# Kernel tuning notes

Hardware: AMD Instinct MI355X
Metric: run time of the kernel (lower is better)

The kernel has to match this reference:

```python
import jax, jax.numpy as jnp
import numpy as np

N_NODES = 100000
N_EDGES = 1600000
IN_CH = 128
HID_CH = 128
OUT_CH = 64
N_GRAPHS = 256


def setup_inputs() -> dict:
    key = jax.random.key(0)
    ks = jax.random.split(key, 12)
    x = jax.random.normal(ks[0], (N_NODES, IN_CH), dtype=jnp.float32)
    edge_index = jax.random.randint(ks[1], (2, N_EDGES), 0, N_NODES, dtype=jnp.int64)
    batch = jnp.sort(jax.random.randint(ks[2], (N_NODES,), 0, N_GRAPHS, dtype=jnp.int64))
    def lin(k, fin, fout):
        bound = 1.0 / np.sqrt(fin)
        kw, kb = jax.random.split(k)
        W = jax.random.uniform(kw, (fin, fout), minval=-bound, maxval=bound, dtype=jnp.float32)
        b = jax.random.uniform(kb, (fout,), minval=-bound, maxval=bound, dtype=jnp.float32)
        return W, b
    W1, b1 = lin(ks[3], IN_CH, HID_CH)
    W2, b2 = lin(ks[4], HID_CH, HID_CH)
    W3, b3 = lin(ks[5], HID_CH, HID_CH)
    Wf, bf = lin(ks[6], HID_CH, OUT_CH)
    return {"x": x, "edge_index": edge_index, "batch": batch,
            "W1": W1, "b1": b1, "W2": W2, "b2": b2,
            "W3": W3, "b3": b3, "Wf": Wf, "bf": bf}


def _gin_conv(x, src, dst, W, b):
    # GINConv with eps=0: nn((1+eps)*x + sum_{j in N(i)} x_j)
    agg = jax.ops.segment_sum(x[src], dst, num_segments=N_NODES)
    return (x + agg) @ W + b


def reference(x, edge_index, batch, W1, b1, W2, b2, W3, b3, Wf, bf):
    src, dst = edge_index[0], edge_index[1]  # source_to_target flow
    h = jax.nn.relu(_gin_conv(x, src, dst, W1, b1))
    h = jax.nn.relu(_gin_conv(h, src, dst, W2, b2))
    h = jax.nn.relu(_gin_conv(h, src, dst, W3, b3))
    # global_mean_pool over graph ids
    sums = jax.ops.segment_sum(h, batch, num_segments=N_GRAPHS)  # [G, H]
    counts = jax.ops.segment_sum(jnp.ones((h.shape[0],), h.dtype), batch, num_segments=N_GRAPHS)
    pooled = sums / jnp.maximum(counts, 1.0)[:, None]
    # dropout is identity in eval mode
    logits = pooled @ Wf + bf  # [G, OUT_CH]
    return logits
```

## Files before the change

### kernel.cpp

```cpp
#include <hip/hip_runtime.h>

#define N_NODES 100000
#define N_EDGES 1600000
#define N_GRAPHS 256
#define CH 128
#define OUT_CH 64
#define NB 391
#define BCAP 4608
#define CAPN 48

typedef __attribute__((ext_vector_type(8))) short bf16x8;
typedef __attribute__((ext_vector_type(4))) float f32x4;
typedef __attribute__((ext_vector_type(2))) float f32x2;
typedef unsigned short ushort_t;
typedef unsigned int uint_t;
typedef unsigned char u8_t;

static __device__ inline ushort_t f2bf(float f) {
    uint_t u = __float_as_uint(f);
    uint_t r = (u + 0x7FFFu + ((u >> 16) & 1u)) >> 16;
    return (ushort_t)r;
}
static __device__ inline uint_t pack2bf(float x, float y) {
    return (uint_t)f2bf(x) | ((uint_t)f2bf(y) << 16);
}

static __device__ inline uint_t pack4fp8(float a, float b, float c, float d) {
    int v = __builtin_amdgcn_cvt_pk_fp8_f32(a, b, 0, false);
    v = __builtin_amdgcn_cvt_pk_fp8_f32(c, d, v, true);
    return (uint_t)v;
}
static __device__ inline u8_t f2fp8(float a) {
    return (u8_t)(__builtin_amdgcn_cvt_pk_fp8_f32(a, a, 0, false) & 0xFF);
}


__global__ __launch_bounds__(1024) void k_passA(const int* __restrict__ src, const int* __restrict__ dst,
                                                int* __restrict__ resCnt, uint_t* __restrict__ pairBuf,
                                                const float* __restrict__ x, u8_t* __restrict__ xb,
                                                const float* __restrict__ W1, const float* __restrict__ W2,
                                                const float* __restrict__ W3, ushort_t* __restrict__ WT) {
    int blk = blockIdx.x, tid = threadIdx.x;
    if (blk < 196) {
        __shared__ int hist[NB];
        __shared__ int base[NB];
        for (int t = tid; t < NB; t += 1024) hist[t] = 0;
        __syncthreads();
        uint_t v[8]; int bk[8], rk[8];
        int e0 = blk * 8192;
        #pragma unroll
        for (int j = 0; j < 8; ++j) {
            int e = e0 + j * 1024 + tid;
            bk[j] = -1;
            if (e < N_EDGES) {
                int d = dst[e];
                int s = src[e];
                int b = d >> 8;
                bk[j] = b;
                v[j] = (uint_t)s | ((uint_t)(d & 255) << 17);
                rk[j] = atomicAdd(&hist[b], 1);
            }
        }
        __syncthreads();
        for (int t = tid; t < NB; t += 1024)
            base[t] = atomicAdd(&resCnt[t * 16], hist[t]);
        __syncthreads();
        #pragma unroll
        for (int j = 0; j < 8; ++j) {
            if (bk[j] >= 0) {
                int pos = base[bk[j]] + rk[j];
                if (pos < BCAP) pairBuf[(size_t)bk[j] * BCAP + pos] = v[j];
            }
        }
    } else if (blk < 1759) {
        int i = (blk - 196) * 1024 + tid;
        if (i < N_NODES * 16) {
            const float4* xp = (const float4*)(x) + (size_t)i * 2;
            float4 a = xp[0], bb = xp[1];
            uint2 o;
            o.x = pack4fp8(a.x, a.y, a.z, a.w);
            o.y = pack4fp8(bb.x, bb.y, bb.z, bb.w);
            ((uint2*)xb)[i] = o;
        }
    } else {
        int idx = (blk - 1759) * 1024 + tid;
        int w = idx >> 14;
        int r = idx & 16383;
        const float* W = (w == 0) ? W1 : (w == 1) ? W2 : W3;
        int k = r >> 7, n = r & 127;
        WT[w * 16384 + n * 128 + k] = f2bf(W[r]);
    }
}


__global__ __launch_bounds__(256) void k_passB(const int* __restrict__ resCnt,
                                               const uint_t* __restrict__ pairBuf,
                                               int* __restrict__ cnt, int* __restrict__ col) {
    __shared__ int csr[256 * CAPN];
    __shared__ int lcnt[256];
    int b = blockIdx.x, tid = threadIdx.x;
    lcnt[tid] = 0;
    for (int i = tid; i < 256 * CAPN; i += 256) csr[i] = 0;
    __syncthreads();
    int ce = resCnt[b * 16];
    if (ce > BCAP) ce = BCAP;
    const uint_t* __restrict__ pb = pairBuf + (size_t)b * BCAP;
    for (int i = tid; i < ce; i += 256) {
        uint_t v = pb[i];
        int d = v >> 17;
        int p = atomicAdd(&lcnt[d], 1);
        if (p < CAPN) csr[d * CAPN + p] = (int)(v & 0x1FFFFu);
    }
    __syncthreads();
    int gbase = b * 256;
    int lim = (gbase + 256 <= N_NODES) ? 256 * CAPN : (N_NODES - gbase) * CAPN;
    for (int i = tid; i < lim; i += 256) col[(size_t)gbase * CAPN + i] = csr[i];
    int node = gbase + tid;
    if (node < N_NODES) {
        int c = lcnt[tid];
        cnt[node] = c > CAPN ? CAPN : c;
    }
}


__global__ __launch_bounds__(1024) void k_sort(const int* __restrict__ cnt, int* __restrict__ perm) {
    __shared__ int hist[CAPN + 1];
    __shared__ int base[CAPN + 1];
    int tid = threadIdx.x;
    if (tid <= CAPN) hist[tid] = 0;
    __syncthreads();
    for (int i = tid; i < N_NODES; i += 1024) atomicAdd(&hist[cnt[i]], 1);
    __syncthreads();
    if (tid == 0) {
        int s = 0;
        for (int b = 0; b <= CAPN; ++b) { base[b] = s; s += hist[b]; }
    }
    __syncthreads();
    for (int i = tid; i < N_NODES; i += 1024) {
        int p = atomicAdd(&base[cnt[i]], 1);
        perm[p] = i;
    }
}


__global__ __launch_bounds__(256) void k_fused(const u8_t* __restrict__ hin,
                                               const int* __restrict__ cnt,
                                               const int* __restrict__ col,
                                               const ushort_t* __restrict__ WT,
                                               const float* __restrict__ bias,
                                               u8_t* __restrict__ Hout,
                                               float* __restrict__ pooled,
                                               const int* __restrict__ batch,
                                               const int* __restrict__ perm) {
    __shared__ uint_t ldsZ[16][68];
    __shared__ float ldsO[16][132];
    __shared__ int ldsP[16];

    int tid  = threadIdx.x;
    int w    = tid >> 6;
    int lane = tid & 63;
    int row0 = blockIdx.x * 16;

    int mrow  = lane & 15;
    int kbase = (lane >> 4) * 8;
    int qid   = lane >> 4;
    int sl    = lane & 15;
    int qb    = qid * 16;

    if (tid < 16) ldsP[tid] = perm ? perm[row0 + tid] : (row0 + tid);

    int prow = row0 + w * 4 + qid;
    int node = perm ? perm[prow] : prow;
    int e = cnt[node];
    int cr0 = col[(size_t)node * CAPN + sl];
    int cr1 = (e > 16) ? col[(size_t)node * CAPN + 16 + sl] : 0;
    int cr2 = (e > 32) ? col[(size_t)node * CAPN + 32 + sl] : 0;

    int emax = e;
    emax = max(emax, __shfl(emax, lane ^ 16));
    emax = max(emax, __shfl(emax, lane ^ 32));

    float f0, f1, f2, f3, f4, f5, f6, f7;
    {
        uint2 sv = *(const uint2*)(hin + (size_t)node * 128 + sl * 8);
        f32x2 p0 = __builtin_amdgcn_cvt_pk_f32_fp8((int)sv.x, false);
        f32x2 p1 = __builtin_amdgcn_cvt_pk_f32_fp8((int)sv.x, true);
        f32x2 p2 = __builtin_amdgcn_cvt_pk_f32_fp8((int)sv.y, false);
        f32x2 p3 = __builtin_amdgcn_cvt_pk_f32_fp8((int)sv.y, true);
        f0 = p0.x; f1 = p0.y; f2 = p1.x; f3 = p1.y;
        f4 = p2.x; f5 = p2.y; f6 = p3.x; f7 = p3.y;
    }

#define ACCG(G, V)                                                       \
    {                                                                    \
        f32x2 p0 = __builtin_amdgcn_cvt_pk_f32_fp8((int)(V).x, false);   \
        f32x2 p1 = __builtin_amdgcn_cvt_pk_f32_fp8((int)(V).x, true);    \
        f32x2 p2 = __builtin_amdgcn_cvt_pk_f32_fp8((int)(V).y, false);   \
        f32x2 p3 = __builtin_amdgcn_cvt_pk_f32_fp8((int)(V).y, true);    \
        f0 = fmaf(G, p0.x, f0); f1 = fmaf(G, p0.y, f1);                  \
        f2 = fmaf(G, p1.x, f2); f3 = fmaf(G, p1.y, f3);                  \
        f4 = fmaf(G, p2.x, f4); f5 = fmaf(G, p2.y, f5);                  \
        f6 = fmaf(G, p3.x, f6); f7 = fmaf(G, p3.y, f7);                  \
    }

#define CHUNK(CREG, BASE)                                                    \
    if ((BASE) < emax) {                                                     \
        int lim = emax - (BASE); if (lim > 16) lim = 16;                     \
        for (int tt = 0; tt < lim; tt += 4) {                                \
            int i1 = tt + 1, i2 = tt + 2, i3 = tt + 3;                       \
            if (i1 > 15) i1 = 15; if (i2 > 15) i2 = 15; if (i3 > 15) i3 = 15;\
            int c0 = __shfl(CREG, qb + tt);                                  \
            int c1 = __shfl(CREG, qb + i1);                                  \
            int c2 = __shfl(CREG, qb + i2);                                  \
            int c3 = __shfl(CREG, qb + i3);                                  \
            bool v0 = (BASE) + tt     < e;                                   \
            bool v1 = (BASE) + tt + 1 < e;                                   \
            bool v2 = (BASE) + tt + 2 < e;                                   \
            bool v3 = (BASE) + tt + 3 < e;                                   \
            int a0 = v0 ? c0 : node;                                         \
            int a1 = v1 ? c1 : node;                                         \
            int a2 = v2 ? c2 : node;                                         \
            int a3 = v3 ? c3 : node;                                         \
            uint2 x0 = *(const uint2*)(hin + (size_t)a0 * 128 + sl * 8);     \
            uint2 x1 = *(const uint2*)(hin + (size_t)a1 * 128 + sl * 8);     \
            uint2 x2 = *(const uint2*)(hin + (size_t)a2 * 128 + sl * 8);     \
            uint2 x3 = *(const uint2*)(hin + (size_t)a3 * 128 + sl * 8);     \
            float g0 = v0 ? 1.0f : 0.0f;                                     \
            float g1 = v1 ? 1.0f : 0.0f;                                     \
            float g2 = v2 ? 1.0f : 0.0f;                                     \
            float g3 = v3 ? 1.0f : 0.0f;                                     \
            ACCG(g0, x0) ACCG(g1, x1) ACCG(g2, x2) ACCG(g3, x3)              \
        }                                                                    \
    }

    CHUNK(cr0, 0)
    CHUNK(cr1, 16)
    CHUNK(cr2, 32)
#undef CHUNK
#undef ACCG

    {
        uint4 o;
        o.x = pack2bf(f0, f1);
        o.y = pack2bf(f2, f3);
        o.z = pack2bf(f4, f5);
        o.w = pack2bf(f6, f7);
        *(uint4*)&ldsZ[w * 4 + qid][sl * 4] = o;
    }

    __builtin_amdgcn_sched_barrier(0);
    bf16x8 bfr[2][4];
    #pragma unroll
    for (int j = 0; j < 2; ++j) {
        int nt = w * 2 + j;
        #pragma unroll
        for (int kc = 0; kc < 4; ++kc) {
            bfr[j][kc] = *(const bf16x8*)(WT + (size_t)(nt * 16 + mrow) * 128 + kc * 32 + kbase);
        }
    }
    __syncthreads();

    f32x4 acc[2];
    #pragma unroll
    for (int j = 0; j < 2; ++j) { f32x4 zz = {0.f, 0.f, 0.f, 0.f}; acc[j] = zz; }

    const ushort_t* zsh = (const ushort_t*)&ldsZ[0][0];
    #pragma unroll
    for (int kc = 0; kc < 4; ++kc) {
        int k0 = kc * 32 + kbase;
        bf16x8 afrag = *(const bf16x8*)(zsh + mrow * 136 + k0);
        acc[0] = __builtin_amdgcn_mfma_f32_16x16x32_bf16(afrag, bfr[0][kc], acc[0], 0, 0, 0);
        acc[1] = __builtin_amdgcn_mfma_f32_16x16x32_bf16(afrag, bfr[1][kc], acc[1], 0, 0, 0);
    }

    int colbase = lane & 15;
    int rsel = (lane >> 4) * 4;

    if (pooled == nullptr) {
        #pragma unroll
        for (int j = 0; j < 2; ++j) {
            int coln = (w * 2 + j) * 16 + colbase;
            float bv = bias[coln];
            #pragma unroll
            for (int r = 0; r < 4; ++r) {
                float v = fmaxf(acc[j][r] + bv, 0.0f);
                int grow = ldsP[rsel + r];
                Hout[(size_t)grow * 128 + coln] = f2fp8(v);
            }
        }
    } else {
        #pragma unroll
        for (int j = 0; j < 2; ++j) {
            int coln = (w * 2 + j) * 16 + colbase;
            float bv = bias[coln];
            #pragma unroll
            for (int r = 0; r < 4; ++r) {
                ldsO[rsel + r][coln] = fmaxf(acc[j][r] + bv, 0.0f);
            }
        }
        __syncthreads();
        if (tid < 128) {
            int gprev = batch[row0];
            float run = 0.f;
            #pragma unroll
            for (int r = 0; r < 16; ++r) {
                int gr = batch[row0 + r];
                if (gr != gprev) {
                    atomicAdd(&pooled[gprev * 128 + tid], run);
                    run = 0.f;
                    gprev = gr;
                }
                run += ldsO[r][tid];
            }
            atomicAdd(&pooled[gprev * 128 + tid], run);
        }
    }
}


__global__ __launch_bounds__(64) void k_final(const float* __restrict__ pooled,
                                              const int* __restrict__ batch,
                                              const float* __restrict__ Wf,
                                              const float* __restrict__ bfv,
                                              float* __restrict__ out) {
    __shared__ float pl[128];
    int g = blockIdx.x, t = threadIdx.x;
    int lo = 0, hi = N_NODES;
    while (lo < hi) { int mid = (lo + hi) >> 1; if (batch[mid] < g) lo = mid + 1; else hi = mid; }
    int s = lo;
    lo = 0; hi = N_NODES;
    while (lo < hi) { int mid = (lo + hi) >> 1; if (batch[mid] < g + 1) lo = mid + 1; else hi = mid; }
    float inv = 1.0f / fmaxf((float)(lo - s), 1.0f);
    pl[t] = pooled[g * 128 + t] * inv;
    pl[t + 64] = pooled[g * 128 + t + 64] * inv;
    __syncthreads();
    float acc = bfv[t];
    #pragma unroll 8
    for (int k = 0; k < CH; ++k) acc += pl[k] * Wf[k * 64 + t];
    out[g * 64 + t] = acc;
}

extern "C" void kernel_launch(void* const* d_in, const int* in_sizes, int n_in,
                              void* d_out, int out_size, void* d_ws, size_t ws_size,
                              hipStream_t stream) {
    const float* x   = (const float*)d_in[0];
    const int*   ei  = (const int*)d_in[1];
    const int*   src = ei;
    const int*   dst = ei + N_EDGES;
    const int*   batch = (const int*)d_in[2];
    const float* W1 = (const float*)d_in[3];
    const float* b1 = (const float*)d_in[4];
    const float* W2 = (const float*)d_in[5];
    const float* b2 = (const float*)d_in[6];
    const float* W3 = (const float*)d_in[7];
    const float* b3 = (const float*)d_in[8];
    const float* Wf = (const float*)d_in[9];
    const float* bf = (const float*)d_in[10];
    float* out = (float*)d_out;

    char* p = (char*)d_ws;
    auto alloc = [&](size_t bytes) -> void* {
        void* r = (void*)p;
        p += (bytes + 255) & ~(size_t)255;
        return r;
    };
    int* resCnt = (int*)alloc((size_t)NB * 16 * sizeof(int));
    float* pooled = (float*)alloc((size_t)N_GRAPHS * CH * sizeof(float));
    size_t zeroBytes = (size_t)((char*)(pooled + N_GRAPHS * CH) - (char*)resCnt);
    uint_t* pairBuf = (uint_t*)alloc((size_t)NB * BCAP * sizeof(uint_t));
    int* cnt = (int*)alloc(N_NODES * sizeof(int));
    int* col = (int*)alloc((size_t)(NB * 256) * CAPN * sizeof(int));
    int* perm = (int*)alloc(N_NODES * sizeof(int));
    ushort_t* wt = (ushort_t*)alloc(3 * CH * CH * sizeof(ushort_t));
    u8_t* xb = (u8_t*)alloc((size_t)N_NODES * CH);
    u8_t* ha = (u8_t*)alloc((size_t)N_NODES * CH);
    u8_t* hb = (u8_t*)alloc((size_t)N_NODES * CH);

    hipMemsetAsync(resCnt, 0, zeroBytes, stream);
    k_passA<<<1807, 1024, 0, stream>>>(src, dst, resCnt, pairBuf, x, xb, W1, W2, W3, wt);
    k_passB<<<NB, 256, 0, stream>>>(resCnt, pairBuf, cnt, col);
    k_sort<<<1, 1024, 0, stream>>>(cnt, perm);

    const int fusedGrid = N_NODES / 16;

    k_fused<<<fusedGrid, 256, 0, stream>>>(xb, cnt, col, wt,         b1, ha, nullptr, nullptr, perm);
    k_fused<<<fusedGrid, 256, 0, stream>>>(ha, cnt, col, wt + 16384, b2, hb, nullptr, nullptr, perm);
    k_fused<<<fusedGrid, 256, 0, stream>>>(hb, cnt, col, wt + 32768, b3, nullptr, pooled, batch, nullptr);
    k_final<<<N_GRAPHS, 64, 0, stream>>>(pooled, batch, Wf, bf, out);
}
```

Measured before the change: 348.7 us.

## Drop degree-sort permutation, widen gather unroll, shrink passA edge blocks

Removes the single-block k_sort kernel and the perm indirection, so the fused layers process nodes in natural order and write outputs directly. The neighbour gather loop now issues 8 loads per iteration instead of 4, for more memory-level parallelism. The edge bucketing in passA uses four times as many blocks, each handling 2048 edges, and skips global atomics for empty histogram bins. The risk is that without degree sorting, wavefronts mix nodes of different degrees and diverge more.

```diff
diff --git a/kernel.cpp b/kernel.cpp
--- a/kernel.cpp
+++ b/kernel.cpp
@@ -41,15 +41,15 @@
                                                 const float* __restrict__ W1, const float* __restrict__ W2,
                                                 const float* __restrict__ W3, ushort_t* __restrict__ WT) {
     int blk = blockIdx.x, tid = threadIdx.x;
-    if (blk < 196) {
+    if (blk < 782) {
         __shared__ int hist[NB];
         __shared__ int base[NB];
         for (int t = tid; t < NB; t += 1024) hist[t] = 0;
         __syncthreads();
-        uint_t v[8]; int bk[8], rk[8];
-        int e0 = blk * 8192;
-        #pragma unroll
-        for (int j = 0; j < 8; ++j) {
+        uint_t v[2]; int bk[2], rk[2];
+        int e0 = blk * 2048;
+        #pragma unroll
+        for (int j = 0; j < 2; ++j) {
             int e = e0 + j * 1024 + tid;
             bk[j] = -1;
             if (e < N_EDGES) {
@@ -62,18 +62,20 @@
             }
         }
         __syncthreads();
-        for (int t = tid; t < NB; t += 1024)
-            base[t] = atomicAdd(&resCnt[t * 16], hist[t]);
+        for (int t = tid; t < NB; t += 1024) {
+            int h = hist[t];
+            if (h) base[t] = atomicAdd(&resCnt[t * 16], h);
+        }
         __syncthreads();
         #pragma unroll
-        for (int j = 0; j < 8; ++j) {
+        for (int j = 0; j < 2; ++j) {
             if (bk[j] >= 0) {
                 int pos = base[bk[j]] + rk[j];
                 if (pos < BCAP) pairBuf[(size_t)bk[j] * BCAP + pos] = v[j];
             }
         }
-    } else if (blk < 1759) {
-        int i = (blk - 196) * 1024 + tid;
+    } else if (blk < 2345) {
+        int i = (blk - 782) * 1024 + tid;
         if (i < N_NODES * 16) {
             const float4* xp = (const float4*)(x) + (size_t)i * 2;
             float4 a = xp[0], bb = xp[1];
@@ -83,7 +85,7 @@
             ((uint2*)xb)[i] = o;
         }
     } else {
-        int idx = (blk - 1759) * 1024 + tid;
+        int idx = (blk - 2345) * 1024 + tid;
         int w = idx >> 14;
         int r = idx & 16383;
         const float* W = (w == 0) ? W1 : (w == 1) ? W2 : W3;
@@ -123,26 +125,6 @@
 }
 
 
-__global__ __launch_bounds__(1024) void k_sort(const int* __restrict__ cnt, int* __restrict__ perm) {
-    __shared__ int hist[CAPN + 1];
-    __shared__ int base[CAPN + 1];
-    int tid = threadIdx.x;
-    if (tid <= CAPN) hist[tid] = 0;
-    __syncthreads();
-    for (int i = tid; i < N_NODES; i += 1024) atomicAdd(&hist[cnt[i]], 1);
-    __syncthreads();
-    if (tid == 0) {
-        int s = 0;
-        for (int b = 0; b <= CAPN; ++b) { base[b] = s; s += hist[b]; }
-    }
-    __syncthreads();
-    for (int i = tid; i < N_NODES; i += 1024) {
-        int p = atomicAdd(&base[cnt[i]], 1);
-        perm[p] = i;
-    }
-}
-
-
 __global__ __launch_bounds__(256) void k_fused(const u8_t* __restrict__ hin,
                                                const int* __restrict__ cnt,
                                                const int* __restrict__ col,
@@ -150,11 +132,9 @@
                                                const float* __restrict__ bias,
                                                u8_t* __restrict__ Hout,
                                                float* __restrict__ pooled,
-                                               const int* __restrict__ batch,
-                                               const int* __restrict__ perm) {
+                                               const int* __restrict__ batch) {
     __shared__ uint_t ldsZ[16][68];
     __shared__ float ldsO[16][132];
-    __shared__ int ldsP[16];
 
     int tid  = threadIdx.x;
     int w    = tid >> 6;
@@ -167,10 +147,7 @@
     int sl    = lane & 15;
     int qb    = qid * 16;
 
-    if (tid < 16) ldsP[tid] = perm ? perm[row0 + tid] : (row0 + tid);
-
-    int prow = row0 + w * 4 + qid;
-    int node = perm ? perm[prow] : prow;
+    int node = row0 + w * 4 + qid;
     int e = cnt[node];
     int cr0 = col[(size_t)node * CAPN + sl];
     int cr1 = (e > 16) ? col[(size_t)node * CAPN + 16 + sl] : 0;
@@ -206,30 +183,22 @@
 #define CHUNK(CREG, BASE)                                                    \
     if ((BASE) < emax) {                                                     \
         int lim = emax - (BASE); if (lim > 16) lim = 16;                     \
-        for (int tt = 0; tt < lim; tt += 4) {                                \
-            int i1 = tt + 1, i2 = tt + 2, i3 = tt + 3;                       \
-            if (i1 > 15) i1 = 15; if (i2 > 15) i2 = 15; if (i3 > 15) i3 = 15;\
-            int c0 = __shfl(CREG, qb + tt);                                  \
-            int c1 = __shfl(CREG, qb + i1);                                  \
-            int c2 = __shfl(CREG, qb + i2);                                  \
-            int c3 = __shfl(CREG, qb + i3);                                  \
-            bool v0 = (BASE) + tt     < e;                                   \
-            bool v1 = (BASE) + tt + 1 < e;                                   \
-            bool v2 = (BASE) + tt + 2 < e;                                   \
-            bool v3 = (BASE) + tt + 3 < e;                                   \
-            int a0 = v0 ? c0 : node;                                         \
-            int a1 = v1 ? c1 : node;                                         \
-            int a2 = v2 ? c2 : node;                                         \
-            int a3 = v3 ? c3 : node;                                         \
-            uint2 x0 = *(const uint2*)(hin + (size_t)a0 * 128 + sl * 8);     \
-            uint2 x1 = *(const uint2*)(hin + (size_t)a1 * 128 + sl * 8);     \
-            uint2 x2 = *(const uint2*)(hin + (size_t)a2 * 128 + sl * 8);     \
-            uint2 x3 = *(const uint2*)(hin + (size_t)a3 * 128 + sl * 8);     \
-            float g0 = v0 ? 1.0f : 0.0f;                                     \
-            float g1 = v1 ? 1.0f : 0.0f;                                     \
-            float g2 = v2 ? 1.0f : 0.0f;                                     \
-            float g3 = v3 ? 1.0f : 0.0f;                                     \
-            ACCG(g0, x0) ACCG(g1, x1) ACCG(g2, x2) ACCG(g3, x3)              \
+        for (int tt = 0; tt < lim; tt += 8) {                                \
+            int c[8]; uint2 xv[8]; float g[8];                               \
+            _Pragma("unroll")                                                \
+            for (int u = 0; u < 8; ++u) {                                    \
+                int iu = tt + u; if (iu > 15) iu = 15;                       \
+                c[u] = __shfl(CREG, qb + iu);                                \
+            }                                                                \
+            _Pragma("unroll")                                                \
+            for (int u = 0; u < 8; ++u) {                                    \
+                bool vu = (BASE) + tt + u < e;                               \
+                int au = vu ? c[u] : node;                                   \
+                g[u] = vu ? 1.0f : 0.0f;                                     \
+                xv[u] = *(const uint2*)(hin + (size_t)au * 128 + sl * 8);    \
+            }                                                                \
+            _Pragma("unroll")                                                \
+            for (int u = 0; u < 8; ++u) { ACCG(g[u], xv[u]) }                \
         }                                                                    \
     }
 
@@ -284,8 +253,7 @@
             #pragma unroll
             for (int r = 0; r < 4; ++r) {
                 float v = fmaxf(acc[j][r] + bv, 0.0f);
-                int grow = ldsP[rsel + r];
-                Hout[(size_t)grow * 128 + coln] = f2fp8(v);
+                Hout[(size_t)(row0 + rsel + r) * 128 + coln] = f2fp8(v);
             }
         }
     } else {
@@ -370,21 +338,19 @@
     uint_t* pairBuf = (uint_t*)alloc((size_t)NB * BCAP * sizeof(uint_t));
     int* cnt = (int*)alloc(N_NODES * sizeof(int));
     int* col = (int*)alloc((size_t)(NB * 256) * CAPN * sizeof(int));
-    int* perm = (int*)alloc(N_NODES * sizeof(int));
     ushort_t* wt = (ushort_t*)alloc(3 * CH * CH * sizeof(ushort_t));
     u8_t* xb = (u8_t*)alloc((size_t)N_NODES * CH);
     u8_t* ha = (u8_t*)alloc((size_t)N_NODES * CH);
     u8_t* hb = (u8_t*)alloc((size_t)N_NODES * CH);
 
     hipMemsetAsync(resCnt, 0, zeroBytes, stream);
-    k_passA<<<1807, 1024, 0, stream>>>(src, dst, resCnt, pairBuf, x, xb, W1, W2, W3, wt);
+    k_passA<<<2393, 1024, 0, stream>>>(src, dst, resCnt, pairBuf, x, xb, W1, W2, W3, wt);
     k_passB<<<NB, 256, 0, stream>>>(resCnt, pairBuf, cnt, col);
-    k_sort<<<1, 1024, 0, stream>>>(cnt, perm);
 
     const int fusedGrid = N_NODES / 16;
 
-    k_fused<<<fusedGrid, 256, 0, stream>>>(xb, cnt, col, wt,         b1, ha, nullptr, nullptr, perm);
-    k_fused<<<fusedGrid, 256, 0, stream>>>(ha, cnt, col, wt + 16384, b2, hb, nullptr, nullptr, perm);
-    k_fused<<<fusedGrid, 256, 0, stream>>>(hb, cnt, col, wt + 32768, b3, nullptr, pooled, batch, nullptr);
+    k_fused<<<fusedGrid, 256, 0, stream>>>(xb, cnt, col, wt,         b1, ha, nullptr, nullptr);
+    k_fused<<<fusedGrid, 256, 0, stream>>>(ha, cnt, col, wt + 16384, b2, hb, nullptr, nullptr);
+    k_fused<<<fusedGrid, 256, 0, stream>>>(hb, cnt, col, wt + 32768, b3, nullptr, pooled, batch);
     k_final<<<N_GRAPHS, 64, 0, stream>>>(pooled, batch, Wf, bf, out);
 }
```

New measurement: 298.7 us. 14.3% less time.
